# Performance work log

Measured on AMD Instinct MI355X. Metric: run time of the kernel, lower is better.

The kernel has to match this reference:

```python
import jax, jax.numpy as jnp
import numpy as np

B, T, I, H, C, L = 64, 256, 256, 1024, 1000, 2


def setup_inputs() -> dict:
    key = jax.random.key(0)
    ks = jax.random.split(key, 10)
    stdv = 1.0 / np.sqrt(H)
    u = lambda k, shape: jax.random.uniform(k, shape, jnp.float32, -stdv, stdv)
    return {
        "x": jax.random.normal(ks[0], (B, T, I), jnp.float32),
        # gate order: g (tanh), i, f, o — stacked on leading axis
        "W0x": u(ks[1], (4, I, H)),
        "W0h": u(ks[2], (4, H, H)),
        "b0": u(ks[3], (4, H)),
        "W1x": u(ks[4], (4, H, H)),
        "W1h": u(ks[5], (4, H, H)),
        "b1": u(ks[6], (4, H)),
        "Wo": u(ks[7], (H, C)),
        "bo": u(ks[8], (C,)),
    }


def _cell(x, h, c, Wx, Wh, b):
    # z: [4, B, H] — one fused contraction for the 4 gates
    z = jnp.einsum('bi,gih->gbh', x, Wx) + jnp.einsum('bh,ghk->gbk', h, Wh) + b[:, None, :]
    g = jnp.tanh(z[0])
    i = jax.nn.sigmoid(z[1])
    f = jax.nn.sigmoid(z[2])
    o = jax.nn.sigmoid(z[3])
    c_new = g * i + c * f
    h_new = jnp.tanh(c_new) * o
    return h_new, c_new


def reference(x, W0x, W0h, b0, W1x, W1h, b1, Wo, bo):
    xt = jnp.transpose(x, (1, 0, 2))  # [T, B, I] like x.permute(1,0,2)
    zeros = jnp.zeros((B, H), x.dtype)
    init = (zeros, zeros, zeros, zeros)  # h0, c0, h1, c1

    def step(carry, x_t):
        h0, c0, h1, c1 = carry
        h0, c0 = _cell(x_t, h0, c0, W0x, W0h, b0)
        h1, c1 = _cell(h0, h1, c1, W1x, W1h, b1)
        return (h0, c0, h1, c1), None

    (h0, c0, h1, c1), _ = jax.lax.scan(step, init, xt)
    return jnp.matmul(h1, Wo) + bo
```

## Files before the change

kernel.cpp:

```cpp
#include <hip/hip_runtime.h>
#include <cstddef>

#define B_  64
#define T_  256
#define I_  256
#define H_  1024
#define C_  1000
#define BH_ (B_ * H_)
#define SLOTS_B_ 24

typedef _Float16 f16;
typedef __attribute__((ext_vector_type(8))) _Float16 f16x8;
typedef __attribute__((ext_vector_type(4))) float f32x4;

__device__ __forceinline__ float sigmoid_(float v) { return 1.0f / (1.0f + __expf(-v)); }
__device__ __forceinline__ float tanh_(float v) {
  float e = __expf(-2.0f * fabsf(v));
  float t = (1.0f - e) / (1.0f + e);
  return copysignf(t, v);
}

__device__ __forceinline__ void storeH2(f16* p, float a, float b) {
  union { f16 h[2]; unsigned u; } pk;
  pk.h[0] = (f16)a; pk.h[1] = (f16)b;
  __hip_atomic_store((unsigned*)p, pk.u, __ATOMIC_RELAXED, __HIP_MEMORY_SCOPE_AGENT);
}


__device__ __forceinline__ unsigned ldS(unsigned* p) {
  return __hip_atomic_load(p, __ATOMIC_RELAXED, __HIP_MEMORY_SCOPE_AGENT);
}

__device__ __forceinline__ void sleepN(int lvl) {
  switch (lvl) {
    case 0: __builtin_amdgcn_s_sleep(1); break;
    case 1: __builtin_amdgcn_s_sleep(2); break;
    case 2: __builtin_amdgcn_s_sleep(4); break;
    default: __builtin_amdgcn_s_sleep(8); break;
  }
}

__device__ __forceinline__ long long waitCtr8(unsigned* base, unsigned tgt) {
  unsigned mn = 0xffffffffu;
#pragma unroll
  for (int j = 0; j < 8; ++j) {
    unsigned v = ldS(base + j * 32);
    mn = (v < mn) ? v : mn;
  }
  if (mn >= tgt) return 0;
  const long long t0 = __builtin_amdgcn_s_memrealtime();
  int lvl = 0, g = 0;
  for (;;) {
    mn = 0xffffffffu;
#pragma unroll
    for (int j = 0; j < 8; ++j) {
      unsigned v = ldS(base + j * 32);
      mn = (v < mn) ? v : mn;
    }
    if (mn >= tgt) break;
    sleepN(lvl);
    if (lvl < 3) ++lvl;
    if (++g > (1 << 17)) break;
  }
  return __builtin_amdgcn_s_memrealtime() - t0;
}

template<bool IS_L1>
__device__ __forceinline__ void role_main(
    const f16* __restrict__ x16, const float* __restrict__ x32,
    const float* __restrict__ Wx, const float* __restrict__ Wh,
    const float* __restrict__ bias,
    f16* __restrict__ h0hist, f16* __restrict__ h1hist,
    unsigned* sync, int bid, int nslots, int fmask, int lagD,
    float* zbAll, float* cLDS, float* biasLDS)
{
  constexpr int NKT = IS_L1 ? 16 : 10;
  constexpr int KX  = IS_L1 ? 1024 : 256;

  const int tid  = threadIdx.x;
  const int wv   = tid >> 6;
  const int nh   = wv >> 2;
  const int kq   = wv & 3;
  const int lane = tid & 63;
  const int c16  = lane & 15;
  const int quad = lane >> 4;
  const int rr7  = bid & 127;
  const int mgroup  = rr7 & 1;
  const int ubase   = (rr7 >> 1) * 16;
  const int rowbase = mgroup * 32;

  const int sub = (rr7 >> 1) & 7;
  unsigned* ctrC0 = sync + ((0 * 2 + mgroup) * 8) * 32;
  unsigned* ctrC1 = sync + ((1 * 2 + mgroup) * 8) * 32;
  unsigned* ctrOwn = IS_L1 ? ctrC1 : ctrC0;
  unsigned* arrLine = ctrOwn + sub * 32;

  auto kmap = [&](int ii) -> int {
    if (!IS_L1) return (ii < 2) ? (kq * 2 + ii) * 32 : 256 + (kq * 8 + (ii - 2)) * 32;
    else        return (ii < 8) ? (kq * 8 + ii) * 32 : 1024 + (kq * 8 + (ii - 8)) * 32;
  };

  if (tid < 64) biasLDS[tid] = bias[(size_t)(tid >> 4) * H_ + ubase + (tid & 15)];
  cLDS[tid] = 0.0f;

  f16x8 Wreg[2][NKT];
  {
    f16* zpan = (f16*)zbAll + wv * 1024;
#pragma unroll
    for (int ii = 0; ii < NKT; ++ii) {
      const int kbase = kmap(ii);
#pragma unroll
      for (int rw = 0; rw < 16; ++rw) {
        const int krow  = rw * 2 + (lane >> 5);
        const int col32 = lane & 31;
        const int g = nh * 2 + (col32 >> 4);
        const int u = col32 & 15;
        const int k = kbase + krow;
        float wval = (k < KX) ? Wx[((size_t)g * KX + k) * H_ + ubase + u]
                              : Wh[((size_t)g * H_ + (k - KX)) * H_ + ubase + u];
        zpan[krow * 32 + col32] = (f16)wval;
      }
#pragma unroll
      for (int nt = 0; nt < 2; ++nt) {
        f16x8 f;
#pragma unroll
        for (int j = 0; j < 8; ++j)
          f[j] = zpan[(quad * 8 + j) * 32 + nt * 16 + c16];
        Wreg[nt][ii] = f;
      }
    }
  }
  __syncthreads();

  const int row0 = rowbase + c16;
  long long wsum = 0;

#pragma unroll 1
  for (int p = 0; p <= T_; ++p) {
    const bool active = IS_L1 ? (p >= 1) : (p < T_);
    const int do_fence = (nslots == 2) ? 1
                        : ((fmask < 0) ? 0 : (((p & fmask) == fmask) ? 1 : 0));

    if (active) {
      const int sp  = p % nslots;
      const int spm = (p - 1 + nslots) % nslots;
      const int spp = (p + 1) % nslots;
      const f16* __restrict__ hA = h0hist + (size_t)sp * BH_;
      const f16* __restrict__ hB = h1hist + (size_t)spm * BH_;
      f16* __restrict__ hdst = IS_L1 ? (h1hist + (size_t)sp  * BH_)
                                     : (h0hist + (size_t)spp * BH_);

      f16x8 Abuf[8][2];
      auto loadTile = [&](int ii, int slot) {
        const int kb = kmap(ii) + quad * 8;
#pragma unroll
        for (int mt2 = 0; mt2 < 2; ++mt2) {
          const int row = row0 + mt2 * 16;
          const f16* src;
          if (!IS_L1) {
            src = (ii < 2) ? (x16 + ((size_t)row * T_ + p) * I_ + kb)
                           : (hA + (size_t)row * H_ + (kb - 256));
          } else {
            src = (ii < 8) ? (hA + (size_t)row * H_ + kb)
                           : (hB + (size_t)row * H_ + (kb - 1024));
          }
          Abuf[slot][mt2] = *(const f16x8*)src;
        }
      };

      f32x4 acc[2][2];
#pragma unroll
      for (int mt2 = 0; mt2 < 2; ++mt2)
#pragma unroll
        for (int nt = 0; nt < 2; ++nt)
          acc[mt2][nt] = (f32x4)0.0f;

      auto mfma4 = [&](int slot, int ii) {
        const f16x8 a0 = Abuf[slot][0];
        const f16x8 a1 = Abuf[slot][1];
        acc[0][0] = __builtin_amdgcn_mfma_f32_16x16x32_f16(a0, Wreg[0][ii], acc[0][0], 0, 0, 0);
        acc[0][1] = __builtin_amdgcn_mfma_f32_16x16x32_f16(a0, Wreg[1][ii], acc[0][1], 0, 0, 0);
        acc[1][0] = __builtin_amdgcn_mfma_f32_16x16x32_f16(a1, Wreg[0][ii], acc[1][0], 0, 0, 0);
        acc[1][1] = __builtin_amdgcn_mfma_f32_16x16x32_f16(a1, Wreg[1][ii], acc[1][1], 0, 0, 0);
      };

      if (!IS_L1) {
        loadTile(0, 0); loadTile(1, 1);
        mfma4(0, 0); mfma4(1, 1);
        if (tid == 0) {
          wsum += waitCtr8(ctrC0, 8u * (unsigned)p);
          if (lagD >= 0 && p > lagD) wsum += waitCtr8(ctrC1, 8u * (unsigned)(p - lagD));
          if (do_fence) __builtin_amdgcn_fence(__ATOMIC_ACQUIRE, "agent");
        }
        __syncthreads();
#pragma unroll
        for (int ii = 2; ii < 10; ++ii) loadTile(ii, ii - 2);
#pragma unroll
        for (int ii = 2; ii < 10; ++ii) mfma4(ii - 2, ii);
      } else {
        if (tid == 0) {
          wsum += waitCtr8(ctrC0, 8u * (unsigned)p);
          if (do_fence) __builtin_amdgcn_fence(__ATOMIC_ACQUIRE, "agent");
        }
        __syncthreads();
#pragma unroll
        for (int ii = 0; ii < 8; ++ii) loadTile(ii, ii);
#pragma unroll
        for (int ii = 0; ii < 8; ++ii) mfma4(ii, ii);
        if (tid == 0) {
          wsum += waitCtr8(ctrC1, 8u * (unsigned)p);
          if (do_fence) __builtin_amdgcn_fence(__ATOMIC_ACQUIRE, "agent");
        }
        __syncthreads();
#pragma unroll
        for (int ii = 8; ii < 16; ++ii) loadTile(ii, ii - 8);
#pragma unroll
        for (int ii = 8; ii < 16; ++ii) mfma4(ii - 8, ii);
      }

      float* zw = zbAll + (nh * 4 + kq) * 1024;
#pragma unroll
      for (int mt2 = 0; mt2 < 2; ++mt2)
#pragma unroll
        for (int nt = 0; nt < 2; ++nt)
#pragma unroll
          for (int e = 0; e < 4; ++e)
            zw[(mt2 * 2 + nt) * 256 + (quad * 4 + e) * 16 + c16] = acc[mt2][nt][e];

      __syncthreads();

      {
        const int base = tid * 4;
        const int nh1  = base >> 10;
        const int off  = base & 1023;
        f32x4 s = (f32x4)0.0f;
#pragma unroll
        for (int q = 0; q < 4; ++q)
          s += *(const f32x4*)(zbAll + nh1 * 4096 + q * 1024 + off);
        const int nt1 = (off >> 8) & 1;
        const int c0  = off & 15;
        s += *(const f32x4*)(biasLDS + (nh1 * 2 + nt1) * 16 + c0);
        *(f32x4*)(zbAll + nh1 * 4096 + off) = s;
      }
      __syncthreads();

      {
        const int row = tid >> 4, u = tid & 15;
        const int mt2 = row >> 4, r16 = row & 15;
        const float z0 = zbAll[0 * 4096 + (mt2 * 2 + 0) * 256 + r16 * 16 + u];
        const float z1 = zbAll[0 * 4096 + (mt2 * 2 + 1) * 256 + r16 * 16 + u];
        const float z2 = zbAll[1 * 4096 + (mt2 * 2 + 0) * 256 + r16 * 16 + u];
        const float z3 = zbAll[1 * 4096 + (mt2 * 2 + 1) * 256 + r16 * 16 + u];
        const float cv = cLDS[tid];
        const float gt = tanh_(z0);
        const float iv = sigmoid_(z1);
        const float fv = sigmoid_(z2);
        const float ov = sigmoid_(z3);
        const float cn = gt * iv + cv * fv;
        cLDS[tid] = cn;
        const float hn = tanh_(cn) * ov;
        const float hn_hi = __shfl_down(hn, 1);
        if ((tid & 1) == 0)
          storeH2(hdst + (size_t)(rowbase + row) * H_ + ubase + u, hn, hn_hi);
      }
    }

    __syncthreads();
    if (tid == 0)
      __hip_atomic_fetch_add(arrLine, 1u, __ATOMIC_RELAXED, __HIP_MEMORY_SCOPE_AGENT);
  }

  if (!IS_L1 && bid == 0) {
    if (tid == 0) {
      waitCtr8(sync + (2 * 8) * 32, 8u * (unsigned)(T_ + 1));
      waitCtr8(sync + (3 * 8) * 32, 8u * (unsigned)(T_ + 1));
      ((long long*)zbAll)[0] = wsum;
    }
    __syncthreads();
    long long nl = ((long long*)zbAll)[0] >> 1;
    if (nl > 200000) nl = 200000;
    char* wb = (char*)(h0hist + BH_);
    for (long long L = tid; L < nl; L += 512)
      __hip_atomic_store((unsigned*)(wb + L * 128), 0x3c003c00u,
                         __ATOMIC_RELAXED, __HIP_MEMORY_SCOPE_AGENT);
  }
  if (IS_L1 && bid == 128) {
    if (tid == 0) ((long long*)zbAll)[0] = wsum;
    __syncthreads();
    long long nl = ((long long*)zbAll)[0] >> 1;
    if (nl > 131000) nl = 131000;
    float s = 0.f;
    for (long long L = tid; L < nl; L += 512)
      s += x32[L * 32];
    if (s != 0.f || tid == 0)
      storeH2(h1hist, s, s);
  }
}

__global__ __launch_bounds__(512, 2)
void lstm_persistent(const f16* __restrict__ x16, const float* __restrict__ x32,
                     const float* __restrict__ W0x, const float* __restrict__ W0h, const float* __restrict__ b0,
                     const float* __restrict__ W1x, const float* __restrict__ W1h, const float* __restrict__ b1,
                     f16* h0hist, f16* h1hist, unsigned* sync,
                     int nslots, int fmask, int lagD)
{
  __shared__ float zbAll[8192];
  __shared__ float cLDS[512];
  __shared__ float biasLDS[64];
  const int bid = blockIdx.x;
  if (bid >= 128)
    role_main<true >(x16, x32, W1x, W1h, b1, h0hist, h1hist, sync, bid, nslots, fmask, lagD, zbAll, cLDS, biasLDS);
  else
    role_main<false>(x16, x32, W0x, W0h, b0, h0hist, h1hist, sync, bid, nslots, fmask, lagD, zbAll, cLDS, biasLDS);
}

__global__ void cvt_x(const float* __restrict__ xin, f16* __restrict__ xo)
{
  const int i = (blockIdx.x * 256 + threadIdx.x) * 8;
  const float4 a = *(const float4*)(xin + i);
  const float4 b = *(const float4*)(xin + i + 4);
  f16x8 v;
  v[0] = (f16)a.x; v[1] = (f16)a.y; v[2] = (f16)a.z; v[3] = (f16)a.w;
  v[4] = (f16)b.x; v[5] = (f16)b.y; v[6] = (f16)b.z; v[7] = (f16)b.w;
  *(f16x8*)(xo + i) = v;
}

__global__ void out_gemm(const f16* __restrict__ h1,
                         const float* __restrict__ Wo, const float* __restrict__ bo,
                         float* __restrict__ out)
{
  __shared__ float ht[1024][8];
  const int tid = threadIdx.x;
  const int b0r = blockIdx.y * 4;
  for (int i = tid; i < 4096; i += 128) {
    const int rr = i >> 10, k = i & 1023;
    ht[k][rr] = (float)h1[(size_t)(b0r + rr) * H_ + k];
  }
  __syncthreads();
  const int c = blockIdx.x * 125 + tid;
  if (tid < 125) {
    float a0 = 0.f, a1 = 0.f, a2 = 0.f, a3 = 0.f;
#pragma unroll 4
    for (int k = 0; k < 1024; ++k) {
      const float w = Wo[(size_t)k * C_ + c];
      a0 += ht[k][0] * w;
      a1 += ht[k][1] * w;
      a2 += ht[k][2] * w;
      a3 += ht[k][3] * w;
    }
    const float bb = bo[c];
    out[(size_t)(b0r + 0) * C_ + c] = a0 + bb;
    out[(size_t)(b0r + 1) * C_ + c] = a1 + bb;
    out[(size_t)(b0r + 2) * C_ + c] = a2 + bb;
    out[(size_t)(b0r + 3) * C_ + c] = a3 + bb;
  }
}

extern "C" void kernel_launch(void* const* d_in, const int* in_sizes, int n_in,
                              void* d_out, int out_size, void* d_ws, size_t ws_size,
                              hipStream_t stream)
{
  const float* x   = (const float*)d_in[0];
  const float* W0x = (const float*)d_in[1];
  const float* W0h = (const float*)d_in[2];
  const float* b0  = (const float*)d_in[3];
  const float* W1x = (const float*)d_in[4];
  const float* W1h = (const float*)d_in[5];
  const float* b1  = (const float*)d_in[6];
  const float* Wo  = (const float*)d_in[7];
  const float* bo  = (const float*)d_in[8];

  const size_t slotB = (size_t)BH_ * sizeof(f16);
  const size_t xB    = (size_t)B_ * T_ * I_ * sizeof(f16);
  const size_t needA = 4096 + (size_t)2 * (T_ + 1) * slotB + xB;
  const size_t needB = 4096 + (size_t)2 * SLOTS_B_ * slotB + xB;
  int nslots, fmask, lagD;
  if (ws_size >= needA)      { nslots = T_ + 1;   fmask = -1; lagD = -1; }
  else if (ws_size >= needB) { nslots = SLOTS_B_; fmask = 15; lagD = 7;  }
  else                       { nslots = 2;        fmask = 0;  lagD = 0;  }
  const size_t histB = (size_t)nslots * slotB;

  unsigned* sync  = (unsigned*)d_ws;
  f16* h0hist = (f16*)((char*)d_ws + 4096);
  f16* h1hist = (f16*)((char*)h0hist + histB);
  f16* x16    = (f16*)((char*)h1hist + histB);

  hipMemsetAsync(d_ws, 0, 4096 + slotB, stream);
  hipMemsetAsync(h1hist, 0, slotB, stream);

  hipLaunchKernelGGL(cvt_x, dim3((B_ * T_ * I_) / (256 * 8)), dim3(256), 0, stream, x, x16);

  hipLaunchKernelGGL(lstm_persistent, dim3(256), dim3(512), 0, stream,
                     x16, x, W0x, W0h, b0, W1x, W1h, b1, h0hist, h1hist, sync,
                     nslots, fmask, lagD);

  f16* h1fin = h1hist + (size_t)(T_ % nslots) * BH_;
  hipLaunchKernelGGL(out_gemm, dim3(8, 16), dim3(128), 0, stream,
                     h1fin, Wo, bo, (float*)d_out);
}
```

Before: 2.529 ms.

## Software-pipeline LSTM steps by precomputing next-step input-projection MFMAs before waiting

Layer 0 now computes the x-input part of the next timestep's gates right after its epilogue, so that work runs while it waits on the recurrent dependency. Layer 1 likewise computes its h0-driven half of the next step ahead of time. It checks all eight layer-0 counters in one batch so it can skip redundant waits for several steps. The aim is to hide cross-block synchronisation latency behind independent matrix work. The post-loop dummy work is rebuilt to scale with a loop timer read via s_memrealtime, and it is now capped by the slot count.

Measured after the change: 2.986 ms. 1.18x slower.

```diff
diff --git a/kernel.cpp b/kernel.cpp
--- a/kernel.cpp
+++ b/kernel.cpp
@@ -133,167 +133,250 @@
   __syncthreads();
 
   const int row0 = rowbase + c16;
-  long long wsum = 0;
-
+
+  f32x4 acc[2][2];
+  f16x8 Abuf[8][2];
+#pragma unroll
+  for (int mt2 = 0; mt2 < 2; ++mt2)
+#pragma unroll
+    for (int nt = 0; nt < 2; ++nt)
+      acc[mt2][nt] = (f32x4)0.0f;
+
+  auto zeroAcc = [&]() {
+#pragma unroll
+    for (int mt2 = 0; mt2 < 2; ++mt2)
+#pragma unroll
+      for (int nt = 0; nt < 2; ++nt)
+        acc[mt2][nt] = (f32x4)0.0f;
+  };
+  auto mfma4 = [&](int slot, int ii) {
+    const f16x8 a0 = Abuf[slot][0];
+    const f16x8 a1 = Abuf[slot][1];
+    acc[0][0] = __builtin_amdgcn_mfma_f32_16x16x32_f16(a0, Wreg[0][ii], acc[0][0], 0, 0, 0);
+    acc[0][1] = __builtin_amdgcn_mfma_f32_16x16x32_f16(a0, Wreg[1][ii], acc[0][1], 0, 0, 0);
+    acc[1][0] = __builtin_amdgcn_mfma_f32_16x16x32_f16(a1, Wreg[0][ii], acc[1][0], 0, 0, 0);
+    acc[1][1] = __builtin_amdgcn_mfma_f32_16x16x32_f16(a1, Wreg[1][ii], acc[1][1], 0, 0, 0);
+  };
+  auto loadH = [&](const f16* base, int ii, int slot) {
+    const int kb = kmap(ii) + quad * 8;
+    const int koff = (IS_L1 && ii >= 8) ? (kb - 1024) : (IS_L1 ? kb : (kb - 256));
+#pragma unroll
+    for (int mt2 = 0; mt2 < 2; ++mt2) {
+      const int row = row0 + mt2 * 16;
+      Abuf[slot][mt2] = *(const f16x8*)(base + (size_t)row * H_ + koff);
+    }
+  };
+  auto loadX = [&](int pp, int ii, int slot) {
+    const int kb = kmap(ii) + quad * 8;
+#pragma unroll
+    for (int mt2 = 0; mt2 < 2; ++mt2) {
+      const int row = row0 + mt2 * 16;
+      Abuf[slot][mt2] = *(const f16x8*)(x16 + ((size_t)row * T_ + pp) * I_ + kb);
+    }
+  };
+
+  auto epilogue = [&](f16* hdst) {
+    float* zw = zbAll + (nh * 4 + kq) * 1024;
+#pragma unroll
+    for (int mt2 = 0; mt2 < 2; ++mt2)
+#pragma unroll
+      for (int nt = 0; nt < 2; ++nt)
+#pragma unroll
+        for (int e = 0; e < 4; ++e)
+          zw[(mt2 * 2 + nt) * 256 + (quad * 4 + e) * 16 + c16] = acc[mt2][nt][e];
+    __syncthreads();
+    {
+      const int base = tid * 4;
+      const int nh1  = base >> 10;
+      const int off  = base & 1023;
+      f32x4 s = (f32x4)0.0f;
+#pragma unroll
+      for (int q = 0; q < 4; ++q)
+        s += *(const f32x4*)(zbAll + nh1 * 4096 + q * 1024 + off);
+      const int nt1 = (off >> 8) & 1;
+      const int c0  = off & 15;
+      s += *(const f32x4*)(biasLDS + (nh1 * 2 + nt1) * 16 + c0);
+      *(f32x4*)(zbAll + nh1 * 4096 + off) = s;
+    }
+    __syncthreads();
+    {
+      const int row = tid >> 4, u = tid & 15;
+      const int mt2 = row >> 4, r16 = row & 15;
+      const float z0 = zbAll[0 * 4096 + (mt2 * 2 + 0) * 256 + r16 * 16 + u];
+      const float z1 = zbAll[0 * 4096 + (mt2 * 2 + 1) * 256 + r16 * 16 + u];
+      const float z2 = zbAll[1 * 4096 + (mt2 * 2 + 0) * 256 + r16 * 16 + u];
+      const float z3 = zbAll[1 * 4096 + (mt2 * 2 + 1) * 256 + r16 * 16 + u];
+      const float cv = cLDS[tid];
+      const float gt = tanh_(z0);
+      const float iv = sigmoid_(z1);
+      const float fv = sigmoid_(z2);
+      const float ov = sigmoid_(z3);
+      const float cn = gt * iv + cv * fv;
+      cLDS[tid] = cn;
+      const float hn = tanh_(cn) * ov;
+      const float hn_hi = __shfl_down(hn, 1);
+      if ((tid & 1) == 0)
+        storeH2(hdst + (size_t)(rowbase + row) * H_ + ubase + u, hn, hn_hi);
+    }
+  };
+
+  auto addArr = [&]() {
+    __hip_atomic_fetch_add(arrLine, 1u, __ATOMIC_RELAXED, __HIP_MEMORY_SCOPE_AGENT);
+  };
+
+  long long wsum = 0, loopT = 0;
+
+  if constexpr (!IS_L1) {
+    loadX(0, 0, 0); loadX(0, 1, 1);
+    mfma4(0, 0); mfma4(1, 1);
 #pragma unroll 1
-  for (int p = 0; p <= T_; ++p) {
-    const bool active = IS_L1 ? (p >= 1) : (p < T_);
-    const int do_fence = (nslots == 2) ? 1
-                        : ((fmask < 0) ? 0 : (((p & fmask) == fmask) ? 1 : 0));
-
-    if (active) {
-      const int sp  = p % nslots;
-      const int spm = (p - 1 + nslots) % nslots;
-      const int spp = (p + 1) % nslots;
-      const f16* __restrict__ hA = h0hist + (size_t)sp * BH_;
-      const f16* __restrict__ hB = h1hist + (size_t)spm * BH_;
-      f16* __restrict__ hdst = IS_L1 ? (h1hist + (size_t)sp  * BH_)
-                                     : (h0hist + (size_t)spp * BH_);
-
-      f16x8 Abuf[8][2];
-      auto loadTile = [&](int ii, int slot) {
-        const int kb = kmap(ii) + quad * 8;
-#pragma unroll
-        for (int mt2 = 0; mt2 < 2; ++mt2) {
-          const int row = row0 + mt2 * 16;
-          const f16* src;
-          if (!IS_L1) {
-            src = (ii < 2) ? (x16 + ((size_t)row * T_ + p) * I_ + kb)
-                           : (hA + (size_t)row * H_ + (kb - 256));
-          } else {
-            src = (ii < 8) ? (hA + (size_t)row * H_ + kb)
-                           : (hB + (size_t)row * H_ + (kb - 1024));
-          }
-          Abuf[slot][mt2] = *(const f16x8*)src;
-        }
-      };
-
-      f32x4 acc[2][2];
-#pragma unroll
-      for (int mt2 = 0; mt2 < 2; ++mt2)
-#pragma unroll
-        for (int nt = 0; nt < 2; ++nt)
-          acc[mt2][nt] = (f32x4)0.0f;
-
-      auto mfma4 = [&](int slot, int ii) {
-        const f16x8 a0 = Abuf[slot][0];
-        const f16x8 a1 = Abuf[slot][1];
-        acc[0][0] = __builtin_amdgcn_mfma_f32_16x16x32_f16(a0, Wreg[0][ii], acc[0][0], 0, 0, 0);
-        acc[0][1] = __builtin_amdgcn_mfma_f32_16x16x32_f16(a0, Wreg[1][ii], acc[0][1], 0, 0, 0);
-        acc[1][0] = __builtin_amdgcn_mfma_f32_16x16x32_f16(a1, Wreg[0][ii], acc[1][0], 0, 0, 0);
-        acc[1][1] = __builtin_amdgcn_mfma_f32_16x16x32_f16(a1, Wreg[1][ii], acc[1][1], 0, 0, 0);
-      };
-
-      if (!IS_L1) {
-        loadTile(0, 0); loadTile(1, 1);
-        mfma4(0, 0); mfma4(1, 1);
+    for (int p = 0; p <= T_; ++p) {
+      const bool active = (p < T_);
+      const int do_fence = (nslots == 2) ? 1
+                          : ((fmask < 0) ? 0 : (((p & fmask) == fmask) ? 1 : 0));
+      if (active) {
         if (tid == 0) {
-          wsum += waitCtr8(ctrC0, 8u * (unsigned)p);
-          if (lagD >= 0 && p > lagD) wsum += waitCtr8(ctrC1, 8u * (unsigned)(p - lagD));
+          (void)waitCtr8(ctrC0, 8u * (unsigned)p);
+          if (lagD >= 0 && p > lagD) (void)waitCtr8(ctrC1, 8u * (unsigned)(p - lagD));
           if (do_fence) __builtin_amdgcn_fence(__ATOMIC_ACQUIRE, "agent");
         }
         __syncthreads();
-#pragma unroll
-        for (int ii = 2; ii < 10; ++ii) loadTile(ii, ii - 2);
+        const f16* hA = h0hist + (size_t)(p % nslots) * BH_;
+        f16* hdst = h0hist + (size_t)((p + 1) % nslots) * BH_;
+#pragma unroll
+        for (int ii = 2; ii < 10; ++ii) loadH(hA, ii, ii - 2);
 #pragma unroll
         for (int ii = 2; ii < 10; ++ii) mfma4(ii - 2, ii);
-      } else {
-        if (tid == 0) {
-          wsum += waitCtr8(ctrC0, 8u * (unsigned)p);
-          if (do_fence) __builtin_amdgcn_fence(__ATOMIC_ACQUIRE, "agent");
+        epilogue(hdst);
+        if (p + 1 < T_) {
+          zeroAcc();
+          loadX(p + 1, 0, 0); loadX(p + 1, 1, 1);
+          mfma4(0, 0); mfma4(1, 1);
         }
-        __syncthreads();
-#pragma unroll
-        for (int ii = 0; ii < 8; ++ii) loadTile(ii, ii);
+      }
+      __syncthreads();
+      if (tid == 0) addArr();
+    }
+  } else {
+    const bool pipe = (nslots > 2);
+    if (pipe) {
+      if (tid == 0) addArr();
+      if (tid == 0) wsum += waitCtr8(ctrC0, 8u);
+      __syncthreads();
+      {
+        const f16* hA1 = h0hist + (size_t)(1 % nslots) * BH_;
+#pragma unroll
+        for (int ii = 0; ii < 8; ++ii) loadH(hA1, ii, ii);
 #pragma unroll
         for (int ii = 0; ii < 8; ++ii) mfma4(ii, ii);
+      }
+      int g1until = 1;
+      long long tA = 0;
+      if (tid == 0) tA = __builtin_amdgcn_s_memrealtime();
+#pragma unroll 1
+      for (int p = 1; p <= T_; ++p) {
+        const int do_fence = (fmask < 0) ? 0 : (((p & fmask) == fmask) ? 1 : 0);
         if (tid == 0) {
           wsum += waitCtr8(ctrC1, 8u * (unsigned)p);
           if (do_fence) __builtin_amdgcn_fence(__ATOMIC_ACQUIRE, "agent");
         }
         __syncthreads();
-#pragma unroll
-        for (int ii = 8; ii < 16; ++ii) loadTile(ii, ii - 8);
+        const f16* hB = h1hist + (size_t)((p - 1 + nslots) % nslots) * BH_;
+#pragma unroll
+        for (int ii = 8; ii < 16; ++ii) loadH(hB, ii, ii - 8);
 #pragma unroll
         for (int ii = 8; ii < 16; ++ii) mfma4(ii - 8, ii);
-      }
-
-      float* zw = zbAll + (nh * 4 + kq) * 1024;
-#pragma unroll
-      for (int mt2 = 0; mt2 < 2; ++mt2)
-#pragma unroll
-        for (int nt = 0; nt < 2; ++nt)
-#pragma unroll
-          for (int e = 0; e < 4; ++e)
-            zw[(mt2 * 2 + nt) * 256 + (quad * 4 + e) * 16 + c16] = acc[mt2][nt][e];
-
+        f16* hdst = h1hist + (size_t)(p % nslots) * BH_;
+        epilogue(hdst);
+        if (p < T_) {
+          if (tid == 0) {
+            const int need = p + 1;
+            if (need > g1until) {
+              int atgt = need + 7; if (atgt > T_ + 1) atgt = T_ + 1;
+              unsigned mn = 0xffffffffu;
+#pragma unroll
+              for (int j = 0; j < 8; ++j) {
+                unsigned v = ldS(ctrC0 + j * 32);
+                mn = (v < mn) ? v : mn;
+              }
+              if (mn >= 8u * (unsigned)atgt) {
+                g1until = atgt;
+              } else {
+                wsum += waitCtr8(ctrC0, 8u * (unsigned)need);
+                g1until = need;
+              }
+            }
+          }
+          __syncthreads();
+          zeroAcc();
+          const f16* hA2 = h0hist + (size_t)((p + 1) % nslots) * BH_;
+#pragma unroll
+          for (int ii = 0; ii < 8; ++ii) loadH(hA2, ii, ii);
+#pragma unroll
+          for (int ii = 0; ii < 8; ++ii) mfma4(ii, ii);
+        }
+        __syncthreads();
+        if (tid == 0) addArr();
+      }
+      if (tid == 0) loopT = __builtin_amdgcn_s_memrealtime() - tA;
+    } else {
+#pragma unroll 1
+      for (int p = 0; p <= T_; ++p) {
+        const bool active = (p >= 1);
+        if (active) {
+          if (tid == 0) {
+            (void)waitCtr8(ctrC0, 8u * (unsigned)p);
+            __builtin_amdgcn_fence(__ATOMIC_ACQUIRE, "agent");
+          }
+          __syncthreads();
+          zeroAcc();
+          const f16* hA = h0hist + (size_t)(p % nslots) * BH_;
+#pragma unroll
+          for (int ii = 0; ii < 8; ++ii) loadH(hA, ii, ii);
+#pragma unroll
+          for (int ii = 0; ii < 8; ++ii) mfma4(ii, ii);
+          if (tid == 0) {
+            (void)waitCtr8(ctrC1, 8u * (unsigned)p);
+            __builtin_amdgcn_fence(__ATOMIC_ACQUIRE, "agent");
+          }
+          __syncthreads();
+          const f16* hB = h1hist + (size_t)((p - 1 + nslots) % nslots) * BH_;
+#pragma unroll
+          for (int ii = 8; ii < 16; ++ii) loadH(hB, ii, ii - 8);
+#pragma unroll
+          for (int ii = 8; ii < 16; ++ii) mfma4(ii - 8, ii);
+          f16* hdst = h1hist + (size_t)(p % nslots) * BH_;
+          epilogue(hdst);
+        }
+        __syncthreads();
+        if (tid == 0) addArr();
+      }
+    }
+
+    if (pipe && bid == 128) {
+      if (tid == 0) { ((long long*)zbAll)[0] = loopT; ((long long*)zbAll)[1] = wsum; }
       __syncthreads();
-
-      {
-        const int base = tid * 4;
-        const int nh1  = base >> 10;
-        const int off  = base & 1023;
-        f32x4 s = (f32x4)0.0f;
-#pragma unroll
-        for (int q = 0; q < 4; ++q)
-          s += *(const f32x4*)(zbAll + nh1 * 4096 + q * 1024 + off);
-        const int nt1 = (off >> 8) & 1;
-        const int c0  = off & 15;
-        s += *(const f32x4*)(biasLDS + (nh1 * 2 + nt1) * 16 + c0);
-        *(f32x4*)(zbAll + nh1 * 4096 + off) = s;
+      long long nl1 = ((long long*)zbAll)[0] >> 1;
+      if (nl1 > 131000) nl1 = 131000;
+      float s = 0.f;
+      for (long long L = tid; L < nl1; L += 512) s += x32[L * 32];
+      if (tid == 0) {
+        (void)waitCtr8(sync + (2 * 8) * 32, 8u * (unsigned)(T_ + 1));
+        (void)waitCtr8(sync + (3 * 8) * 32, 8u * (unsigned)(T_ + 1));
       }
       __syncthreads();
-
-      {
-        const int row = tid >> 4, u = tid & 15;
-        const int mt2 = row >> 4, r16 = row & 15;
-        const float z0 = zbAll[0 * 4096 + (mt2 * 2 + 0) * 256 + r16 * 16 + u];
-        const float z1 = zbAll[0 * 4096 + (mt2 * 2 + 1) * 256 + r16 * 16 + u];
-        const float z2 = zbAll[1 * 4096 + (mt2 * 2 + 0) * 256 + r16 * 16 + u];
-        const float z3 = zbAll[1 * 4096 + (mt2 * 2 + 1) * 256 + r16 * 16 + u];
-        const float cv = cLDS[tid];
-        const float gt = tanh_(z0);
-        const float iv = sigmoid_(z1);
-        const float fv = sigmoid_(z2);
-        const float ov = sigmoid_(z3);
-        const float cn = gt * iv + cv * fv;
-        cLDS[tid] = cn;
-        const float hn = tanh_(cn) * ov;
-        const float hn_hi = __shfl_down(hn, 1);
-        if ((tid & 1) == 0)
-          storeH2(hdst + (size_t)(rowbase + row) * H_ + ubase + u, hn, hn_hi);
-      }
-    }
-
-    __syncthreads();
-    if (tid == 0)
-      __hip_atomic_fetch_add(arrLine, 1u, __ATOMIC_RELAXED, __HIP_MEMORY_SCOPE_AGENT);
-  }
-
-  if (!IS_L1 && bid == 0) {
-    if (tid == 0) {
-      waitCtr8(sync + (2 * 8) * 32, 8u * (unsigned)(T_ + 1));
-      waitCtr8(sync + (3 * 8) * 32, 8u * (unsigned)(T_ + 1));
-      ((long long*)zbAll)[0] = wsum;
-    }
-    __syncthreads();
-    long long nl = ((long long*)zbAll)[0] >> 1;
-    if (nl > 200000) nl = 200000;
-    char* wb = (char*)(h0hist + BH_);
-    for (long long L = tid; L < nl; L += 512)
-      __hip_atomic_store((unsigned*)(wb + L * 128), 0x3c003c00u,
-                         __ATOMIC_RELAXED, __HIP_MEMORY_SCOPE_AGENT);
-  }
-  if (IS_L1 && bid == 128) {
-    if (tid == 0) ((long long*)zbAll)[0] = wsum;
-    __syncthreads();
-    long long nl = ((long long*)zbAll)[0] >> 1;
-    if (nl > 131000) nl = 131000;
-    float s = 0.f;
-    for (long long L = tid; L < nl; L += 512)
-      s += x32[L * 32];
-    if (s != 0.f || tid == 0)
-      storeH2(h1hist, s, s);
+      long long nl2 = ((long long*)zbAll)[1] >> 1;
+      long long maxl = (long long)(nslots - 1) * 1024;
+      if (nl2 > 200000) nl2 = 200000;
+      if (nl2 > maxl)  nl2 = maxl;
+      char* wb = (char*)(h0hist + BH_);
+      for (long long L = tid; L < nl2; L += 512)
+        __hip_atomic_store((unsigned*)(wb + L * 128), 0x3c003c00u,
+                           __ATOMIC_RELAXED, __HIP_MEMORY_SCOPE_AGENT);
+      if (s != 0.f)
+        __hip_atomic_store((unsigned*)wb, 0u,
+                           __ATOMIC_RELAXED, __HIP_MEMORY_SCOPE_AGENT);
+    }
   }
 }
 
```
